# Kernel optimization log

Measured on AMD Instinct MI355X. Metric: run time of the kernel, lower is better.

## Reference

```python
import jax, jax.numpy as jnp
import numpy as np

N_ATOMS, N_EDGES, FEAT, N_RBF, N_CONV = 20000, 320000, 128, 20, 3
CUTOFF = 5.0
ATOM_FEA, H_FEA, N_OUT, VOCAB = 64, 128, 5, 100


def _dense(x, W, b):
    return x @ W + b


def _painn_forward(xyz, embed, W1, b1, W2, b2, Wd, bd, U, V, Ws1, bs1, Ws2, bs2,
                   Wr1, br1, Wr2, br2, Wf1, bf1, Wf2, bf2, Wf3, bf3, z, nbrs):
    act = jax.nn.silu
    i_idx, j_idx = nbrs[:, 0], nbrs[:, 1]          # receiver i, sender j
    r_ij = xyz[j_idx] - xyz[i_idx]                 # [E,3]
    d = jnp.sqrt(jnp.sum(r_ij ** 2, -1) + 1e-12)   # [E]
    unit = r_ij / d[:, None]
    n = jnp.arange(1, N_RBF + 1, dtype=xyz.dtype)
    rbf = jnp.sin(n[None, :] * jnp.pi * d[:, None] / CUTOFF) / d[:, None]   # [E,n_rbf]
    f_cut = 0.5 * (jnp.cos(jnp.pi * d / CUTOFF) + 1.0) * (d < CUTOFF)       # cosine envelope

    s = embed[z]                                   # [N,F]
    v = jnp.zeros((s.shape[0], FEAT, 3), s.dtype)  # [N,F,3]

    for l in range(N_CONV):
        # ---- message block ----
        phi = _dense(act(_dense(s, W1[l], b1[l])), W2[l], b2[l])        # [N,3F]
        w_s = _dense(rbf, Wd[l], bd[l]) * f_cut[:, None]                # [E,3F]
        inv = (phi[j_idx] * w_s).reshape(-1, 3, FEAT)                   # [E,3,F]
        dv_ij = unit[:, None, :] * inv[:, 2, :, None] + inv[:, 0, :, None] * v[j_idx]  # [E,F,3]
        s = s + jax.ops.segment_sum(inv[:, 1, :], i_idx, num_segments=N_ATOMS)
        v = v + jax.ops.segment_sum(dv_ij, i_idx, num_segments=N_ATOMS)
        # ---- update block ----
        u_v = jnp.einsum('nfd,fg->ngd', v, U[l])                        # [N,F,3]
        v_v = jnp.einsum('nfd,fg->ngd', v, V[l])
        v_norm = jnp.sqrt(jnp.sum(v_v ** 2, -1) + 1e-12)                # [N,F]
        split = _dense(act(_dense(jnp.concatenate([s, v_norm], -1), Ws1[l], bs1[l])), Ws2[l], bs2[l])
        a_vv = split[:, :FEAT]
        a_sv = split[:, FEAT:2 * FEAT]
        a_ss = split[:, 2 * FEAT:]
        v = v + u_v * a_vv[:, :, None]
        s = s + jnp.sum(u_v * v_v, -1) * a_sv + a_ss

    # ---- readout (per-atom features) + fully connected head ----
    atom_fea = _dense(act(_dense(s, Wr1, br1)), Wr2, br2)               # [N,atom_fea]
    h = act(_dense(atom_fea, Wf1, bf1))
    h = act(_dense(h, Wf2, bf2))
    return _dense(h, Wf3, bf3)                                          # [N,n_outputs]


def setup_inputs() -> dict:
    key = jax.random.key(0)
    ks = jax.random.split(key, 20)
    sc = 0.08  # ~1/sqrt(feat_dim) to keep activations stable
    def rn(k, shape, s=sc):
        return jax.random.normal(k, shape, dtype=jnp.float32) * s
    return {
        'xyz': jax.random.uniform(ks[0], (N_ATOMS, 3), dtype=jnp.float32) * 4.0,
        'z': jax.random.randint(ks[1], (N_ATOMS,), 0, VOCAB),
        'nbrs': jax.random.randint(ks[2], (N_EDGES, 2), 0, N_ATOMS),
        'embed': rn(ks[3], (VOCAB, FEAT), 1.0),
        'W1': rn(ks[4], (N_CONV, FEAT, FEAT)), 'b1': jnp.zeros((N_CONV, FEAT)),
        'W2': rn(ks[5], (N_CONV, FEAT, 3 * FEAT)), 'b2': jnp.zeros((N_CONV, 3 * FEAT)),
        'Wd': rn(ks[6], (N_CONV, N_RBF, 3 * FEAT)), 'bd': jnp.zeros((N_CONV, 3 * FEAT)),
        'U': rn(ks[7], (N_CONV, FEAT, FEAT)),
        'V': rn(ks[8], (N_CONV, FEAT, FEAT)),
        'Ws1': rn(ks[9], (N_CONV, 2 * FEAT, FEAT)), 'bs1': jnp.zeros((N_CONV, FEAT)),
        'Ws2': rn(ks[10], (N_CONV, FEAT, 3 * FEAT)), 'bs2': jnp.zeros((N_CONV, 3 * FEAT)),
        'Wr1': rn(ks[11], (FEAT, FEAT)), 'br1': jnp.zeros((FEAT,)),
        'Wr2': rn(ks[12], (FEAT, ATOM_FEA)), 'br2': jnp.zeros((ATOM_FEA,)),
        'Wf1': rn(ks[13], (ATOM_FEA, H_FEA)), 'bf1': jnp.zeros((H_FEA,)),
        'Wf2': rn(ks[14], (H_FEA, H_FEA)), 'bf2': jnp.zeros((H_FEA,)),
        'Wf3': rn(ks[15], (H_FEA, N_OUT)), 'bf3': jnp.zeros((N_OUT,)),
    }


def reference(xyz, z, nbrs, embed, W1, b1, W2, b2, Wd, bd, U, V, Ws1, bs1, Ws2, bs2,
              Wr1, br1, Wr2, br2, Wf1, bf1, Wf2, bf2, Wf3, bf3):
    return _painn_forward(xyz, embed, W1, b1, W2, b2, Wd, bd, U, V, Ws1, bs1, Ws2, bs2,
                          Wr1, br1, Wr2, br2, Wf1, bf1, Wf2, bf2, Wf3, bf3, z, nbrs)
```

## Files before the change

kernel.cpp:

```cpp
#include <hip/hip_runtime.h>
#include <hip/hip_bf16.h>
#include <math.h>

#define N_ATOMS 20000
#define N_EDGES 320000
#define FEAT 128
#define N_RBF 20
#define N_CONV 3
#define N_OUT_ 5
#define PI_F 3.14159265358979f
#define M20P 20032
#define M60P 60032

typedef unsigned short ushort;
typedef __bf16 bf16x8 __attribute__((ext_vector_type(8)));
typedef float f32x4 __attribute__((ext_vector_type(4)));

__device__ __forceinline__ float b2f(ushort u){ return __uint_as_float(((unsigned)u) << 16); }
__device__ __forceinline__ ushort f2b(float x){
    unsigned u = __float_as_uint(x);
    return (ushort)((u + 0x7FFFu + ((u >> 16) & 1u)) >> 16);
}
#define MFMA __builtin_amdgcn_mfma_f32_16x16x32_bf16

constexpr size_t rnd64(size_t x){ return (x + 63) & ~size_t(63); }
constexpr size_t F_XYZ  = 64;
constexpr size_t F_EMB  = rnd64(F_XYZ + 60000);
constexpr size_t F_B1   = rnd64(F_EMB + 12800);
constexpr size_t F_B2   = rnd64(F_B1  + 3*128);
constexpr size_t F_WD   = rnd64(F_B2  + 3*384);
constexpr size_t F_BD   = rnd64(F_WD  + 3*20*384);
constexpr size_t F_BS1  = rnd64(F_BD  + 3*384);
constexpr size_t F_BS2  = rnd64(F_BS1 + 3*128);
constexpr size_t F_BR1  = rnd64(F_BS2 + 3*384);
constexpr size_t F_BR2  = rnd64(F_BR1 + 128);
constexpr size_t F_BF1  = rnd64(F_BR2 + 64);
constexpr size_t F_BF2  = rnd64(F_BF1 + 128);
constexpr size_t F_BF3  = rnd64(F_BF2 + 128);
constexpr size_t F_CNT  = rnd64(F_BF3 + 8);
constexpr size_t F_ROW  = rnd64(F_CNT  + N_ATOMS);
constexpr size_t F_CUR  = rnd64(F_ROW  + N_ATOMS + 1);
constexpr size_t F_EID  = rnd64(F_CUR  + N_ATOMS);
constexpr size_t F_EJ   = rnd64(F_EID  + N_EDGES);
constexpr size_t F_EREC = rnd64(F_EJ   + N_EDGES);
constexpr size_t F_S    = rnd64(F_EREC + (size_t)N_EDGES*24);
constexpr size_t F_V    = rnd64(F_S    + (size_t)N_ATOMS*FEAT);
constexpr size_t F_PHI  = rnd64(F_V    + (size_t)60000*FEAT);
constexpr size_t F_VV   = rnd64(F_PHI  + (size_t)N_ATOMS*384);
constexpr size_t F_SPL  = rnd64(F_VV   + (size_t)60000*FEAT);
constexpr size_t F_OUT  = rnd64(F_SPL  + (size_t)N_ATOMS*384);
constexpr size_t H_SHI  = rnd64(F_OUT  + N_ATOMS*N_OUT_);
constexpr size_t H_SLO  = rnd64(H_SHI  + (size_t)M20P*128/2);
constexpr size_t H_VHI  = rnd64(H_SLO  + (size_t)M20P*128/2);
constexpr size_t H_VLO  = rnd64(H_VHI  + (size_t)M60P*128/2);
constexpr size_t H_HAHI = rnd64(H_VLO  + (size_t)M60P*128/2);
constexpr size_t H_HALO = rnd64(H_HAHI + (size_t)M20P*128/2);
constexpr size_t H_HBHI = rnd64(H_HALO + (size_t)M20P*128/2);
constexpr size_t H_HBLO = rnd64(H_HBHI + (size_t)M20P*128/2);
constexpr size_t H_AFHI = rnd64(H_HBLO + (size_t)M20P*128/2);
constexpr size_t H_AFLO = rnd64(H_AFHI + (size_t)M20P*64/2);
constexpr size_t H_WT   = rnd64(H_AFLO + (size_t)M20P*64/2);
constexpr size_t O_W1T=0, O_W2T=49152, O_UT=196608, O_VT=245760, O_WS1T=294912,
                 O_WS2T=393216, O_WR1T=540672, O_WR2T=557056, O_WF1T=565248,
                 O_WF2T=573440, O_WF3T=589824, O_WTOT=598016;

__global__ void k_detect(const unsigned int* __restrict__ bits, int* flag){
    __shared__ int cnt;
    if (threadIdx.x == 0) cnt = 0;
    __syncthreads();
    unsigned int lo = bits[threadIdx.x] & 0xFFFFu;
    if (lo >= 0x3000u && lo <= 0x4100u) atomicAdd(&cnt, 1);
    __syncthreads();
    if (threadIdx.x == 0) *flag = (cnt >= 48) ? 1 : 0;
}

struct P13 { const void* p[13]; };
__global__ void k_cvt_all(P13 sp, float* __restrict__ ws, const int* __restrict__ flag){
    constexpr int   NSEG = 13;
    constexpr int    SZ[NSEG] = {60000,12800,384,1152,23040,1152,384,1152,128,64,128,128,5};
    constexpr size_t DO_[NSEG]= {F_XYZ,F_EMB,F_B1,F_B2,F_WD,F_BD,F_BS1,F_BS2,F_BR1,F_BR2,F_BF1,F_BF2,F_BF3};
    int t = blockIdx.x * blockDim.x + threadIdx.x;
    int bf = *flag;
    #pragma unroll
    for (int s = 0; s < NSEG; s++){
        if (t < SZ[s]){
            float v = bf ? b2f(((const ushort*)sp.p[s])[t]) : ((const float*)sp.p[s])[t];
            ws[DO_[s] + t] = v;
            return;
        }
        t -= SZ[s];
    }
}

struct P11 { const void* p[11]; };
__global__ void k_wt_all(P11 sp, ushort* __restrict__ wb, const int* __restrict__ flag){
    constexpr int NSEG = 23;
    constexpr int SRC[NSEG]  = {0,1,2,3,4,5, 0,1,2,3,4,5, 0,1,2,3,4,5, 6,7,8,9,10};
    constexpr int SOFF[NSEG] = {0,0,0,0,0,0, 16384,49152,16384,16384,32768,49152,
                                32768,98304,32768,32768,65536,98304, 0,0,0,0,0};
    constexpr size_t DOFF[NSEG]={O_W1T,O_W2T,O_UT,O_VT,O_WS1T,O_WS2T,
                                 O_W1T+16384,O_W2T+49152,O_UT+16384,O_VT+16384,O_WS1T+32768,O_WS2T+49152,
                                 O_W1T+32768,O_W2T+98304,O_UT+32768,O_VT+32768,O_WS1T+65536,O_WS2T+98304,
                                 O_WR1T,O_WR2T,O_WF1T,O_WF2T,O_WF3T};
    constexpr int KK[NSEG]   = {128,128,128,128,256,128, 128,128,128,128,256,128,
                                128,128,128,128,256,128, 128,128,64,128,128};
    constexpr int NN[NSEG]   = {128,384,128,128,128,384, 128,384,128,128,128,384,
                                128,384,128,128,128,384, 128,64,128,128,5};
    constexpr int NP[NSEG]   = {128,384,128,128,128,384, 128,384,128,128,128,384,
                                128,384,128,128,128,384, 128,64,128,128,64};
    constexpr int PM[NSEG]   = {0,0,0,0,0,1, 0,0,0,0,0,1, 0,0,0,0,0,1, 0,0,0,0,0};
    int t = blockIdx.x * blockDim.x + threadIdx.x;
    int bf = *flag;
    #pragma unroll
    for (int s = 0; s < NSEG; s++){
        int tot = NP[s] * KK[s];
        if (t < tot){
            int n = t / KK[s], k = t & (KK[s] - 1);
            ushort hi = 0, lo = 0;
            if (n < NN[s]){
                int si = SOFF[s] + k * NN[s] + n;
                float w = bf ? b2f(((const ushort*)sp.p[SRC[s]])[si])
                             : ((const float*)sp.p[SRC[s]])[si];
                hi = f2b(w); lo = f2b(w - b2f(hi));
            }
            int dr = n;
            if (PM[s]) { int g = n & 127, tg = n >> 7; dr = (g >> 6) * 192 + tg * 64 + (g & 63); }
            size_t di = DOFF[s] + (size_t)dr * KK[s] + k;
            wb[di] = hi;
            wb[O_WTOT + di] = lo;
            return;
        }
        t -= tot;
    }
}
constexpr int WT_TOTAL = 598016;

__global__ void k_store_out(const float* __restrict__ src, void* __restrict__ dst, int n,
                            const int* __restrict__ flag){
    int t = blockIdx.x * blockDim.x + threadIdx.x;
    if (t >= n) return;
    float v = src[t];
    if (*flag) ((ushort*)dst)[t] = f2b(v);
    else       ((float*)dst)[t] = v;
}

__global__ void k_zero_f(float* p, int n){
    int t = blockIdx.x * blockDim.x + threadIdx.x;
    if (t < n) p[t] = 0.f;
}
__global__ void k_zero_i(int* p, int n){
    int t = blockIdx.x * blockDim.x + threadIdx.x;
    if (t < n) p[t] = 0;
}
__global__ void k_init_s(const float* __restrict__ embed, const int* __restrict__ z,
                         float* __restrict__ s, ushort* __restrict__ shi,
                         ushort* __restrict__ slo){
    int t = blockIdx.x * blockDim.x + threadIdx.x;
    if (t >= N_ATOMS * FEAT) return;
    int n = t >> 7, f = t & 127;
    float v = embed[z[n] * FEAT + f];
    s[t] = v;
    ushort h = f2b(v); shi[t] = h; slo[t] = f2b(v - b2f(h));
}

__global__ void k_hist(const int* __restrict__ nbrs, int* __restrict__ cnt){
    int e = blockIdx.x * blockDim.x + threadIdx.x;
    if (e < N_EDGES) atomicAdd(&cnt[nbrs[2*e]], 1);
}
__global__ void k_scan(const int* __restrict__ cnt, int* __restrict__ row, int* __restrict__ cur){
    __shared__ int ls[256];
    int t = threadIdx.x, base = t * 80;
    int s = 0;
    for (int k = 0; k < 80; k++){ int i = base + k; if (i < N_ATOMS) s += cnt[i]; }
    ls[t] = s; __syncthreads();
    for (int off = 1; off < 256; off <<= 1){
        int v = (t >= off) ? ls[t - off] : 0;
        __syncthreads();
        ls[t] += v;
        __syncthreads();
    }
    int run = ls[t] - s;
    for (int k = 0; k < 80; k++){
        int i = base + k;
        if (i < N_ATOMS){ row[i] = run; cur[i] = run; run += cnt[i]; }
    }
    if (t == 255) row[N_ATOMS] = ls[255];
}
__global__ void k_fill(const int* __restrict__ nbrs, int* __restrict__ cur, int* __restrict__ eid){
    int e = blockIdx.x * blockDim.x + threadIdx.x;
    if (e >= N_EDGES) return;
    int p = atomicAdd(&cur[nbrs[2*e]], 1);
    eid[p] = e;
}

__global__ void k_geom_csr(const float* __restrict__ xyz, const int* __restrict__ nbrs,
                           const int* __restrict__ eid,
                           int* __restrict__ EJ, float* __restrict__ EREC){
    int idx = blockIdx.x * blockDim.x + threadIdx.x;
    if (idx >= N_EDGES) return;
    int e = eid[idx];
    int i = nbrs[2*e], j = nbrs[2*e+1];
    float rx = xyz[3*j]   - xyz[3*i];
    float ry = xyz[3*j+1] - xyz[3*i+1];
    float rz = xyz[3*j+2] - xyz[3*i+2];
    float d  = sqrtf(rx*rx + ry*ry + rz*rz + 1e-12f);
    float inv = 1.0f / d;
    float b  = PI_F * d * 0.2f;
    float sb = sinf(b), cb = cosf(b);
    float fc = (d < 5.0f) ? 0.5f * (cb + 1.0f) : 0.0f;
    float scale = inv * fc, c2 = 2.0f * cb;
    EJ[idx] = j;
    float* rec = EREC + (size_t)idx * 24;
    rec[0] = fc; rec[1] = rx*inv; rec[2] = ry*inv; rec[3] = rz*inv;
    float sp = 0.f, sc = sb;
    #pragma unroll
    for (int r = 0; r < N_RBF; r++){
        rec[4 + r] = sc * scale;
        float sn = c2 * sc - sp;
        sp = sc; sc = sn;
    }
}

template<int KT>
__global__ __launch_bounds__(256) void k_gemm3t(
    const ushort* __restrict__ Ahi, const ushort* __restrict__ Alo,
    const ushort* __restrict__ Bthi, const ushort* __restrict__ Btlo,
    const float* __restrict__ bias, int M, int N, int act,
    float* __restrict__ Cf, ushort* __restrict__ Chi, ushort* __restrict__ Clo)
{
    int wave = threadIdx.x >> 6, lane = threadIdx.x & 63;
    int l15 = lane & 15, quad = lane >> 4;
    int m0 = blockIdx.y * 128 + wave * 32;
    int n0 = blockIdx.x * 64;
    const ushort* aph = Ahi  + (size_t)(m0 + l15) * KT + quad * 8;
    const ushort* apl = Alo  + (size_t)(m0 + l15) * KT + quad * 8;
    const ushort* bph = Bthi + (size_t)(n0 + l15) * KT + quad * 8;
    const ushort* bpl = Btlo + (size_t)(n0 + l15) * KT + quad * 8;
    f32x4 acc[2][4];
    #pragma unroll
    for (int r = 0; r < 2; r++)
        #pragma unroll
        for (int c = 0; c < 4; c++) acc[r][c] = (f32x4){0.f, 0.f, 0.f, 0.f};
    #pragma unroll
    for (int k0 = 0; k0 < KT; k0 += 32) {
        bf16x8 ah0 = *reinterpret_cast<const bf16x8*>(aph + k0);
        bf16x8 al0 = *reinterpret_cast<const bf16x8*>(apl + k0);
        bf16x8 ah1 = *reinterpret_cast<const bf16x8*>(aph + (size_t)16 * KT + k0);
        bf16x8 al1 = *reinterpret_cast<const bf16x8*>(apl + (size_t)16 * KT + k0);
        #pragma unroll
        for (int c = 0; c < 4; c++) {
            bf16x8 bh = *reinterpret_cast<const bf16x8*>(bph + (size_t)c * 16 * KT + k0);
            bf16x8 bl = *reinterpret_cast<const bf16x8*>(bpl + (size_t)c * 16 * KT + k0);
            acc[0][c] = MFMA(al0, bh, acc[0][c], 0, 0, 0);
            acc[0][c] = MFMA(ah0, bl, acc[0][c], 0, 0, 0);
            acc[0][c] = MFMA(ah0, bh, acc[0][c], 0, 0, 0);
            acc[1][c] = MFMA(al1, bh, acc[1][c], 0, 0, 0);
            acc[1][c] = MFMA(ah1, bl, acc[1][c], 0, 0, 0);
            acc[1][c] = MFMA(ah1, bh, acc[1][c], 0, 0, 0);
        }
    }
    #pragma unroll
    for (int rr = 0; rr < 2; rr++) {
        int row_base = m0 + rr * 16 + quad * 4;
        #pragma unroll
        for (int c = 0; c < 4; c++) {
            int col = n0 + c * 16 + l15;
            #pragma unroll
            for (int r = 0; r < 4; r++) {
                int row = row_base + r;
                if (row < M && col < N) {
                    float v = acc[rr][c][r];
                    if (bias) v += bias[col];
                    if (act)  v = v / (1.f + expf(-v));
                    size_t idx = (size_t)row * N + col;
                    if (Cf)  Cf[idx] = v;
                    if (Chi) { ushort h = f2b(v); Chi[idx] = h; Clo[idx] = f2b(v - b2f(h)); }
                }
            }
        }
    }
}

__global__ __launch_bounds__(256) void k_gemm3_dual(
    const ushort* __restrict__ Ahi, const ushort* __restrict__ Alo,
    const ushort* __restrict__ B1hi, const ushort* __restrict__ B1lo,
    const ushort* __restrict__ B2hi, const ushort* __restrict__ B2lo,
    int M, float* __restrict__ C1, float* __restrict__ C2)
{
    constexpr int KT = 128, N = 128;
    int wave = threadIdx.x >> 6, lane = threadIdx.x & 63;
    int l15 = lane & 15, quad = lane >> 4;
    int m0 = blockIdx.y * 128 + wave * 32;
    int n0 = blockIdx.x * 64;
    const ushort* aph = Ahi  + (size_t)(m0 + l15) * KT + quad * 8;
    const ushort* apl = Alo  + (size_t)(m0 + l15) * KT + quad * 8;
    const ushort* b1h = B1hi + (size_t)(n0 + l15) * KT + quad * 8;
    const ushort* b1l = B1lo + (size_t)(n0 + l15) * KT + quad * 8;
    const ushort* b2h = B2hi + (size_t)(n0 + l15) * KT + quad * 8;
    const ushort* b2l = B2lo + (size_t)(n0 + l15) * KT + quad * 8;
    f32x4 acc1[2][4], acc2[2][4];
    #pragma unroll
    for (int r = 0; r < 2; r++)
        #pragma unroll
        for (int c = 0; c < 4; c++) {
            acc1[r][c] = (f32x4){0.f,0.f,0.f,0.f};
            acc2[r][c] = (f32x4){0.f,0.f,0.f,0.f};
        }
    #pragma unroll
    for (int k0 = 0; k0 < KT; k0 += 32) {
        bf16x8 ah0 = *reinterpret_cast<const bf16x8*>(aph + k0);
        bf16x8 al0 = *reinterpret_cast<const bf16x8*>(apl + k0);
        bf16x8 ah1 = *reinterpret_cast<const bf16x8*>(aph + (size_t)16 * KT + k0);
        bf16x8 al1 = *reinterpret_cast<const bf16x8*>(apl + (size_t)16 * KT + k0);
        #pragma unroll
        for (int c = 0; c < 4; c++) {
            bf16x8 bh = *reinterpret_cast<const bf16x8*>(b1h + (size_t)c * 16 * KT + k0);
            bf16x8 bl = *reinterpret_cast<const bf16x8*>(b1l + (size_t)c * 16 * KT + k0);
            acc1[0][c] = MFMA(al0, bh, acc1[0][c], 0, 0, 0);
            acc1[0][c] = MFMA(ah0, bl, acc1[0][c], 0, 0, 0);
            acc1[0][c] = MFMA(ah0, bh, acc1[0][c], 0, 0, 0);
            acc1[1][c] = MFMA(al1, bh, acc1[1][c], 0, 0, 0);
            acc1[1][c] = MFMA(ah1, bl, acc1[1][c], 0, 0, 0);
            acc1[1][c] = MFMA(ah1, bh, acc1[1][c], 0, 0, 0);
        }
        #pragma unroll
        for (int c = 0; c < 4; c++) {
            bf16x8 bh = *reinterpret_cast<const bf16x8*>(b2h + (size_t)c * 16 * KT + k0);
            bf16x8 bl = *reinterpret_cast<const bf16x8*>(b2l + (size_t)c * 16 * KT + k0);
            acc2[0][c] = MFMA(al0, bh, acc2[0][c], 0, 0, 0);
            acc2[0][c] = MFMA(ah0, bl, acc2[0][c], 0, 0, 0);
            acc2[0][c] = MFMA(ah0, bh, acc2[0][c], 0, 0, 0);
            acc2[1][c] = MFMA(al1, bh, acc2[1][c], 0, 0, 0);
            acc2[1][c] = MFMA(ah1, bl, acc2[1][c], 0, 0, 0);
            acc2[1][c] = MFMA(ah1, bh, acc2[1][c], 0, 0, 0);
        }
    }
    #pragma unroll
    for (int rr = 0; rr < 2; rr++) {
        int row_base = m0 + rr * 16 + quad * 4;
        #pragma unroll
        for (int c = 0; c < 4; c++) {
            int col = n0 + c * 16 + l15;
            #pragma unroll
            for (int r = 0; r < 4; r++) {
                int row = row_base + r;
                if (row < M) {
                    size_t idx = (size_t)row * N + col;
                    C1[idx] = acc1[rr][c][r];
                    C2[idx] = acc2[rr][c][r];
                }
            }
        }
    }
}

__global__ __launch_bounds__(384) void k_ws2up(
    const ushort* __restrict__ Ahi, const ushort* __restrict__ Alo,
    const ushort* __restrict__ Bphi, const ushort* __restrict__ Bplo,
    const float* __restrict__ bs2,
    const float* __restrict__ uv, const float* __restrict__ vvf,
    const ushort* __restrict__ vhi, const ushort* __restrict__ vlo,
    float* __restrict__ s, float* __restrict__ v,
    ushort* __restrict__ shi, ushort* __restrict__ slo, int M)
{
    constexpr int KT = 128, LDG = 200;
    __shared__ float gl[64 * LDG];
    int wave = threadIdx.x >> 6, lane = threadIdx.x & 63;
    int l15 = lane & 15, quad = lane >> 4;
    int tg = wave >> 1, rh = wave & 1;
    int m0 = blockIdx.y * 64 + rh * 32;
    int X  = blockIdx.x;
    const ushort* aph = Ahi  + (size_t)(m0 + l15) * KT + quad * 8;
    const ushort* apl = Alo  + (size_t)(m0 + l15) * KT + quad * 8;
    const ushort* bph = Bphi + (size_t)(X * 192 + tg * 64 + l15) * KT + quad * 8;
    const ushort* bpl = Bplo + (size_t)(X * 192 + tg * 64 + l15) * KT + quad * 8;
    f32x4 acc[2][4];
    #pragma unroll
    for (int r = 0; r < 2; r++)
        #pragma unroll
        for (int c = 0; c < 4; c++) acc[r][c] = (f32x4){0.f, 0.f, 0.f, 0.f};
    #pragma unroll
    for (int k0 = 0; k0 < KT; k0 += 32) {
        bf16x8 ah0 = *reinterpret_cast<const bf16x8*>(aph + k0);
        bf16x8 al0 = *reinterpret_cast<const bf16x8*>(apl + k0);
        bf16x8 ah1 = *reinterpret_cast<const bf16x8*>(aph + (size_t)16 * KT + k0);
        bf16x8 al1 = *reinterpret_cast<const bf16x8*>(apl + (size_t)16 * KT + k0);
        #pragma unroll
        for (int c = 0; c < 4; c++) {
            bf16x8 bh = *reinterpret_cast<const bf16x8*>(bph + (size_t)c * 16 * KT + k0);
            bf16x8 bl = *reinterpret_cast<const bf16x8*>(bpl + (size_t)c * 16 * KT + k0);
            acc[0][c] = MFMA(al0, bh, acc[0][c], 0, 0, 0);
            acc[0][c] = MFMA(ah0, bl, acc[0][c], 0, 0, 0);
            acc[0][c] = MFMA(ah0, bh, acc[0][c], 0, 0, 0);
            acc[1][c] = MFMA(al1, bh, acc[1][c], 0, 0, 0);
            acc[1][c] = MFMA(ah1, bl, acc[1][c], 0, 0, 0);
            acc[1][c] = MFMA(ah1, bh, acc[1][c], 0, 0, 0);
        }
    }
    #pragma unroll
    for (int rr = 0; rr < 2; rr++) {
        #pragma unroll
        for (int c = 0; c < 4; c++) {
            #pragma unroll
            for (int r = 0; r < 4; r++) {
                int lrow = rh * 32 + rr * 16 + quad * 4 + r;
                int gc   = c * 16 + l15;
                gl[lrow * LDG + tg * 64 + gc] = acc[rr][c][r] + bs2[tg * 128 + X * 64 + gc];
            }
        }
    }
    __syncthreads();
    int a0 = blockIdx.y * 64;
    for (int t = threadIdx.x; t < 64 * 64; t += 384) {
        int al = t >> 6, gc = t & 63;
        int a = a0 + al;
        if (a >= M) continue;
        int g = X * 64 + gc;
        float avv = gl[al * LDG + gc];
        float asv = gl[al * LDG + 64 + gc];
        float ass = gl[al * LDG + 128 + gc];
        size_t b = (size_t)a * 384 + g;
        float dot = 0.f;
        #pragma unroll
        for (int d = 0; d < 3; d++) {
            size_t idx = b + (size_t)d * 128;
            float u  = uv[idx];
            float w  = vvf[idx];
            float vb = b2f(vhi[idx]) + b2f(vlo[idx]);
            dot = fmaf(u, w, dot);
            v[idx] = vb + u * avv;
        }
        size_t st = (size_t)a * FEAT + g;
        float ns = s[st] + dot * asv + ass;
        s[st] = ns;
        ushort h = f2b(ns); shi[st] = h; slo[st] = f2b(ns - b2f(h));
    }
}

__global__ __launch_bounds__(128) void k_edge4(
    const float* __restrict__ phi, const float* __restrict__ vin,
    const int* __restrict__ EJ, const float* __restrict__ EREC,
    const int* __restrict__ row,
    const float* __restrict__ Wd, const float* __restrict__ bd,
    float* __restrict__ s, ushort* __restrict__ vhi, ushort* __restrict__ vlo)
{
    int i = blockIdx.x, f = threadIdx.x;
    float wdr[3 * N_RBF];
    #pragma unroll
    for (int r = 0; r < N_RBF; r++) {
        wdr[r]           = Wd[r*384 + f];
        wdr[N_RBF + r]   = Wd[r*384 + 128 + f];
        wdr[2*N_RBF + r] = Wd[r*384 + 256 + f];
    }
    float bd0 = bd[f], bd1 = bd[128 + f], bd2 = bd[256 + f];
    float sacc = 0.f, va0 = 0.f, va1 = 0.f, va2 = 0.f;
    int beg = row[i], end = row[i + 1];

    auto body = [&](int idx){
        int j = EJ[idx];
        const float4* rq = reinterpret_cast<const float4*>(EREC + (size_t)idx * 24);
        float4 q0 = rq[0], q1 = rq[1], q2 = rq[2], q3 = rq[3], q4 = rq[4], q5 = rq[5];
        float g[20] = {q1.x,q1.y,q1.z,q1.w, q2.x,q2.y,q2.z,q2.w,
                       q3.x,q3.y,q3.z,q3.w, q4.x,q4.y,q4.z,q4.w,
                       q5.x,q5.y,q5.z,q5.w};
        float w0 = bd0 * q0.x, w1 = bd1 * q0.x, w2 = bd2 * q0.x;
        #pragma unroll
        for (int r = 0; r < N_RBF; r++) {
            w0 = fmaf(g[r], wdr[r],           w0);
            w1 = fmaf(g[r], wdr[N_RBF + r],   w1);
            w2 = fmaf(g[r], wdr[2*N_RBF + r], w2);
        }
        size_t pj = (size_t)j * 384;
        float inv0 = phi[pj + f]       * w0;
        float inv1 = phi[pj + 128 + f] * w1;
        float inv2 = phi[pj + 256 + f] * w2;
        size_t vj = (size_t)j * 384 + f;
        sacc += inv1;
        va0 = fmaf(inv0, vin[vj],       fmaf(q0.y, inv2, va0));
        va1 = fmaf(inv0, vin[vj + 128], fmaf(q0.z, inv2, va1));
        va2 = fmaf(inv0, vin[vj + 256], fmaf(q0.w, inv2, va2));
    };

    int idx = beg;
    for (; idx + 1 < end; idx += 2) { body(idx); body(idx + 1); }
    if (idx < end) body(idx);

    s[(size_t)i * FEAT + f] += sacc;
    size_t vi = (size_t)i * 384 + f;
    float n0 = vin[vi] + va0, n1 = vin[vi + 128] + va1, n2 = vin[vi + 256] + va2;
    ushort h;
    h = f2b(n0); vhi[vi]       = h; vlo[vi]       = f2b(n0 - b2f(h));
    h = f2b(n1); vhi[vi + 128] = h; vlo[vi + 128] = f2b(n1 - b2f(h));
    h = f2b(n2); vhi[vi + 256] = h; vlo[vi + 256] = f2b(n2 - b2f(h));
}

__global__ void k_vnorm_cat(const float* __restrict__ s, const float* __restrict__ vv,
                            ushort* __restrict__ chi, ushort* __restrict__ clo){
    int t = blockIdx.x * blockDim.x + threadIdx.x;
    if (t >= N_ATOMS * FEAT) return;
    int n = t >> 7, g = t & 127;
    size_t b = (size_t)n * 384 + g;
    float a0 = vv[b], a1 = vv[b + 128], a2 = vv[b + 256];
    float nr = sqrtf(a0*a0 + a1*a1 + a2*a2 + 1e-12f);
    float sv = s[t];
    size_t c0 = (size_t)n * 256 + g;
    ushort h;
    h = f2b(sv); chi[c0]       = h; clo[c0]       = f2b(sv - b2f(h));
    h = f2b(nr); chi[c0 + 128] = h; clo[c0 + 128] = f2b(nr - b2f(h));
}

struct Pair { ushort* hi; ushort* lo; };

static inline void gemm3(Pair A, Pair B, const float* bias,
                         int M, int K, int N, int Npad, int act,
                         float* Cf, Pair C, hipStream_t s){
    dim3 g(Npad / 64, (M + 127) / 128), b(256);
    switch (K) {
    case 64:  k_gemm3t<64> <<<g, b, 0, s>>>(A.hi, A.lo, B.hi, B.lo, bias, M, N, act, Cf, C.hi, C.lo); break;
    case 128: k_gemm3t<128><<<g, b, 0, s>>>(A.hi, A.lo, B.hi, B.lo, bias, M, N, act, Cf, C.hi, C.lo); break;
    case 256: k_gemm3t<256><<<g, b, 0, s>>>(A.hi, A.lo, B.hi, B.lo, bias, M, N, act, Cf, C.hi, C.lo); break;
    }
}

extern "C" void kernel_launch(void* const* d_in, const int* in_sizes, int n_in,
                              void* d_out, int out_size, void* d_ws, size_t ws_size,
                              hipStream_t stream) {
    float* ws = (float*)d_ws;
    int* flag = (int*)d_ws;
    const int* z    = (const int*)d_in[1];
    const int* nbrs = (const int*)d_in[2];

    k_detect<<<1, 64, 0, stream>>>((const unsigned int*)d_in[0], flag);

    P13 cp; {
        const int cidx[13] = {0,3,5,7,8,9,13,15,17,19,21,23,25};
        for (int i = 0; i < 13; i++) cp.p[i] = d_in[cidx[i]];
    }
    k_cvt_all<<<(100517 + 255)/256, 256, 0, stream>>>(cp, ws, flag);

    ushort* wb = (ushort*)(ws + H_WT);
    P11 wp; {
        const int widx[11] = {4,6,10,11,12,14,16,18,20,22,24};
        for (int i = 0; i < 11; i++) wp.p[i] = d_in[widx[i]];
    }
    k_wt_all<<<(WT_TOTAL + 255)/256, 256, 0, stream>>>(wp, wb, flag);

    int* cnt = (int*)(ws + F_CNT); int* row = (int*)(ws + F_ROW);
    int* cur = (int*)(ws + F_CUR); int* eid = (int*)(ws + F_EID);
    int* EJ  = (int*)(ws + F_EJ);  float* EREC = ws + F_EREC;
    k_zero_i<<<(N_ATOMS+255)/256, 256, 0, stream>>>(cnt, N_ATOMS);
    k_hist<<<(N_EDGES+255)/256, 256, 0, stream>>>(nbrs, cnt);
    k_scan<<<1, 256, 0, stream>>>(cnt, row, cur);
    k_fill<<<(N_EDGES+255)/256, 256, 0, stream>>>(nbrs, cur, eid);
    k_geom_csr<<<(N_EDGES+255)/256, 256, 0, stream>>>(ws + F_XYZ, nbrs, eid, EJ, EREC);

    float* S   = ws + F_S;
    float* V   = ws + F_V;
    float* PHI = ws + F_PHI;
    float* VV  = ws + F_VV;
    Pair SHL { (ushort*)(ws + H_SHI),  (ushort*)(ws + H_SLO)  };
    Pair VHL { (ushort*)(ws + H_VHI),  (ushort*)(ws + H_VLO)  };
    Pair HA  { (ushort*)(ws + H_HAHI), (ushort*)(ws + H_HALO) };
    Pair HB  { (ushort*)(ws + H_HBHI), (ushort*)(ws + H_HBLO) };
    Pair AF  { (ushort*)(ws + H_AFHI), (ushort*)(ws + H_AFLO) };
    Pair CAT { (ushort*)(ws + F_SPL),  (ushort*)(ws + F_SPL) + (size_t)M20P*256 };
    Pair NOP { nullptr, nullptr };

    k_init_s<<<(N_ATOMS*FEAT+255)/256, 256, 0, stream>>>(ws + F_EMB, z, S, SHL.hi, SHL.lo);
    k_zero_f<<<(60000*FEAT+255)/256, 256, 0, stream>>>(V, 60000*FEAT);

    for (int l = 0; l < N_CONV; l++) {
        gemm3(SHL, Pair{wb + O_W1T + l*16384, wb + O_WTOT + O_W1T + l*16384},
              ws + F_B1 + l*128, N_ATOMS, 128, 128, 128, 1, nullptr, HA, stream);
        gemm3(HA, Pair{wb + O_W2T + l*49152, wb + O_WTOT + O_W2T + l*49152},
              ws + F_B2 + l*384, N_ATOMS, 128, 384, 384, 0, PHI, NOP, stream);
        k_edge4<<<N_ATOMS, 128, 0, stream>>>(PHI, V, EJ, EREC, row,
                                             ws + F_WD + (size_t)l*20*384, ws + F_BD + l*384,
                                             S, VHL.hi, VHL.lo);
        {
            dim3 g(2, (60000 + 127) / 128), b(256);
            k_gemm3_dual<<<g, b, 0, stream>>>(VHL.hi, VHL.lo,
                                              wb + O_UT + l*16384, wb + O_WTOT + O_UT + l*16384,
                                              wb + O_VT + l*16384, wb + O_WTOT + O_VT + l*16384,
                                              60000, PHI, VV);
        }
        k_vnorm_cat<<<(N_ATOMS*FEAT+255)/256, 256, 0, stream>>>(S, VV, CAT.hi, CAT.lo);
        gemm3(CAT, Pair{wb + O_WS1T + l*32768, wb + O_WTOT + O_WS1T + l*32768},
              ws + F_BS1 + l*128, N_ATOMS, 256, 128, 128, 1, nullptr, HB, stream);
        {
            dim3 g(2, (N_ATOMS + 63) / 64), b(384);
            k_ws2up<<<g, b, 0, stream>>>(HB.hi, HB.lo,
                                         wb + O_WS2T + l*49152, wb + O_WTOT + O_WS2T + l*49152,
                                         ws + F_BS2 + l*384,
                                         PHI, VV, VHL.hi, VHL.lo,
                                         S, V, SHL.hi, SHL.lo, N_ATOMS);
        }
    }

    gemm3(SHL, Pair{wb + O_WR1T, wb + O_WTOT + O_WR1T}, ws + F_BR1,
          N_ATOMS, 128, 128, 128, 1, nullptr, HA, stream);
    gemm3(HA,  Pair{wb + O_WR2T, wb + O_WTOT + O_WR2T}, ws + F_BR2,
          N_ATOMS, 128,  64,  64, 0, nullptr, AF, stream);
    gemm3(AF,  Pair{wb + O_WF1T, wb + O_WTOT + O_WF1T}, ws + F_BF1,
          N_ATOMS,  64, 128, 128, 1, nullptr, HB, stream);
    gemm3(HB,  Pair{wb + O_WF2T, wb + O_WTOT + O_WF2T}, ws + F_BF2,
          N_ATOMS, 128, 128, 128, 1, nullptr, HA, stream);
    gemm3(HA,  Pair{wb + O_WF3T, wb + O_WTOT + O_WF3T}, ws + F_BF3,
          N_ATOMS, 128, N_OUT_, 64, 0, ws + F_OUT, NOP, stream);

    k_store_out<<<(N_ATOMS*N_OUT_+255)/256, 256, 0, stream>>>(ws + F_OUT, d_out, N_ATOMS*N_OUT_, flag);
}
```

Baseline: 1.343 ms.

## Fuse vector-norm/concat into dual U/V GEMM and skip zero-v reads on first layer

The dual U/V GEMM now tiles rows in steps of 126, so each block holds whole atoms (42 atoms of 3 rows). It stages the V-projection tile in shared memory and computes the per-atom vector norm plus the split bf16 concat with s inline, which removes the separate k_vnorm_cat pass and its reread of VV. The edge kernel is templated so the first layer skips reading the all-zero v, which also removes the zeroing kernel. The cost is overlapping tiles (128 rows computed per 126 used), some wasted MFMA work, a larger padded V buffer, and 35KB of shared memory per block.

```diff
diff --git a/kernel.cpp b/kernel.cpp
--- a/kernel.cpp
+++ b/kernel.cpp
@@ -10,7 +10,7 @@
 #define N_OUT_ 5
 #define PI_F 3.14159265358979f
 #define M20P 20032
-#define M60P 60032
+#define M60PAD 60160
 
 typedef unsigned short ushort;
 typedef __bf16 bf16x8 __attribute__((ext_vector_type(8)));
@@ -52,8 +52,8 @@
 constexpr size_t H_SHI  = rnd64(F_OUT  + N_ATOMS*N_OUT_);
 constexpr size_t H_SLO  = rnd64(H_SHI  + (size_t)M20P*128/2);
 constexpr size_t H_VHI  = rnd64(H_SLO  + (size_t)M20P*128/2);
-constexpr size_t H_VLO  = rnd64(H_VHI  + (size_t)M60P*128/2);
-constexpr size_t H_HAHI = rnd64(H_VLO  + (size_t)M60P*128/2);
+constexpr size_t H_VLO  = rnd64(H_VHI  + (size_t)M60PAD*128/2);
+constexpr size_t H_HAHI = rnd64(H_VLO  + (size_t)M60PAD*128/2);
 constexpr size_t H_HALO = rnd64(H_HAHI + (size_t)M20P*128/2);
 constexpr size_t H_HBHI = rnd64(H_HALO + (size_t)M20P*128/2);
 constexpr size_t H_HBLO = rnd64(H_HBHI + (size_t)M20P*128/2);
@@ -144,10 +144,6 @@
     else       ((float*)dst)[t] = v;
 }
 
-__global__ void k_zero_f(float* p, int n){
-    int t = blockIdx.x * blockDim.x + threadIdx.x;
-    if (t < n) p[t] = 0.f;
-}
 __global__ void k_zero_i(int* p, int n){
     int t = blockIdx.x * blockDim.x + threadIdx.x;
     if (t < n) p[t] = 0;
@@ -281,16 +277,19 @@
     }
 }
 
-__global__ __launch_bounds__(256) void k_gemm3_dual(
+__global__ __launch_bounds__(256) void k_dual_vn(
     const ushort* __restrict__ Ahi, const ushort* __restrict__ Alo,
     const ushort* __restrict__ B1hi, const ushort* __restrict__ B1lo,
     const ushort* __restrict__ B2hi, const ushort* __restrict__ B2lo,
-    int M, float* __restrict__ C1, float* __restrict__ C2)
+    const float* __restrict__ s,
+    float* __restrict__ C1, float* __restrict__ C2,
+    ushort* __restrict__ chi, ushort* __restrict__ clo)
 {
-    constexpr int KT = 128, N = 128;
+    constexpr int KT = 128, N = 128, MROWS = 60000, LDV = 68;
+    __shared__ float vvs[128 * LDV];
     int wave = threadIdx.x >> 6, lane = threadIdx.x & 63;
     int l15 = lane & 15, quad = lane >> 4;
-    int m0 = blockIdx.y * 128 + wave * 32;
+    int m0 = blockIdx.y * 126 + wave * 32;
     int n0 = blockIdx.x * 64;
     const ushort* aph = Ahi  + (size_t)(m0 + l15) * KT + quad * 8;
     const ushort* apl = Alo  + (size_t)(m0 + l15) * KT + quad * 8;
@@ -337,20 +336,39 @@
     }
     #pragma unroll
     for (int rr = 0; rr < 2; rr++) {
-        int row_base = m0 + rr * 16 + quad * 4;
         #pragma unroll
         for (int c = 0; c < 4; c++) {
             int col = n0 + c * 16 + l15;
             #pragma unroll
             for (int r = 0; r < 4; r++) {
-                int row = row_base + r;
-                if (row < M) {
+                int lrow = wave * 32 + rr * 16 + quad * 4 + r;
+                int row  = m0 + rr * 16 + quad * 4 + r;
+                float vv = acc2[rr][c][r];
+                vvs[lrow * LDV + c * 16 + l15] = vv;
+                if (row < MROWS) {
                     size_t idx = (size_t)row * N + col;
                     C1[idx] = acc1[rr][c][r];
-                    C2[idx] = acc2[rr][c][r];
+                    C2[idx] = vv;
                 }
             }
         }
+    }
+    __syncthreads();
+    int a0 = blockIdx.y * 42;
+    for (int t = threadIdx.x; t < 42 * 64; t += 256) {
+        int a_loc = t >> 6, c = t & 63;
+        int a = a0 + a_loc;
+        if (a >= N_ATOMS) continue;
+        float v0 = vvs[(a_loc * 3 + 0) * LDV + c];
+        float v1 = vvs[(a_loc * 3 + 1) * LDV + c];
+        float v2 = vvs[(a_loc * 3 + 2) * LDV + c];
+        float nr = sqrtf(v0 * v0 + v1 * v1 + v2 * v2 + 1e-12f);
+        int g = n0 + c;
+        float sv = s[(size_t)a * FEAT + g];
+        size_t c0 = (size_t)a * 256 + g;
+        ushort h;
+        h = f2b(sv); chi[c0]       = h; clo[c0]       = f2b(sv - b2f(h));
+        h = f2b(nr); chi[c0 + 128] = h; clo[c0 + 128] = f2b(nr - b2f(h));
     }
 }
 
@@ -437,7 +455,8 @@
     }
 }
 
-__global__ __launch_bounds__(128) void k_edge4(
+template<int FIRST>
+__global__ __launch_bounds__(128) void k_edge4t(
     const float* __restrict__ phi, const float* __restrict__ vin,
     const int* __restrict__ EJ, const float* __restrict__ EREC,
     const int* __restrict__ row,
@@ -474,11 +493,17 @@
         float inv0 = phi[pj + f]       * w0;
         float inv1 = phi[pj + 128 + f] * w1;
         float inv2 = phi[pj + 256 + f] * w2;
-        size_t vj = (size_t)j * 384 + f;
         sacc += inv1;
-        va0 = fmaf(inv0, vin[vj],       fmaf(q0.y, inv2, va0));
-        va1 = fmaf(inv0, vin[vj + 128], fmaf(q0.z, inv2, va1));
-        va2 = fmaf(inv0, vin[vj + 256], fmaf(q0.w, inv2, va2));
+        if (FIRST) {
+            va0 = fmaf(q0.y, inv2, va0);
+            va1 = fmaf(q0.z, inv2, va1);
+            va2 = fmaf(q0.w, inv2, va2);
+        } else {
+            size_t vj = (size_t)j * 384 + f;
+            va0 = fmaf(inv0, vin[vj],       fmaf(q0.y, inv2, va0));
+            va1 = fmaf(inv0, vin[vj + 128], fmaf(q0.z, inv2, va1));
+            va2 = fmaf(inv0, vin[vj + 256], fmaf(q0.w, inv2, va2));
+        }
     };
 
     int idx = beg;
@@ -487,26 +512,13 @@
 
     s[(size_t)i * FEAT + f] += sacc;
     size_t vi = (size_t)i * 384 + f;
-    float n0 = vin[vi] + va0, n1 = vin[vi + 128] + va1, n2 = vin[vi + 256] + va2;
+    float n0, n1, n2;
+    if (FIRST) { n0 = va0; n1 = va1; n2 = va2; }
+    else { n0 = vin[vi] + va0; n1 = vin[vi + 128] + va1; n2 = vin[vi + 256] + va2; }
     ushort h;
     h = f2b(n0); vhi[vi]       = h; vlo[vi]       = f2b(n0 - b2f(h));
     h = f2b(n1); vhi[vi + 128] = h; vlo[vi + 128] = f2b(n1 - b2f(h));
     h = f2b(n2); vhi[vi + 256] = h; vlo[vi + 256] = f2b(n2 - b2f(h));
-}
-
-__global__ void k_vnorm_cat(const float* __restrict__ s, const float* __restrict__ vv,
-                            ushort* __restrict__ chi, ushort* __restrict__ clo){
-    int t = blockIdx.x * blockDim.x + threadIdx.x;
-    if (t >= N_ATOMS * FEAT) return;
-    int n = t >> 7, g = t & 127;
-    size_t b = (size_t)n * 384 + g;
-    float a0 = vv[b], a1 = vv[b + 128], a2 = vv[b + 256];
-    float nr = sqrtf(a0*a0 + a1*a1 + a2*a2 + 1e-12f);
-    float sv = s[t];
-    size_t c0 = (size_t)n * 256 + g;
-    ushort h;
-    h = f2b(sv); chi[c0]       = h; clo[c0]       = f2b(sv - b2f(h));
-    h = f2b(nr); chi[c0 + 128] = h; clo[c0 + 128] = f2b(nr - b2f(h));
 }
 
 struct Pair { ushort* hi; ushort* lo; };
@@ -567,24 +579,25 @@
     Pair NOP { nullptr, nullptr };
 
     k_init_s<<<(N_ATOMS*FEAT+255)/256, 256, 0, stream>>>(ws + F_EMB, z, S, SHL.hi, SHL.lo);
-    k_zero_f<<<(60000*FEAT+255)/256, 256, 0, stream>>>(V, 60000*FEAT);
 
     for (int l = 0; l < N_CONV; l++) {
         gemm3(SHL, Pair{wb + O_W1T + l*16384, wb + O_WTOT + O_W1T + l*16384},
               ws + F_B1 + l*128, N_ATOMS, 128, 128, 128, 1, nullptr, HA, stream);
         gemm3(HA, Pair{wb + O_W2T + l*49152, wb + O_WTOT + O_W2T + l*49152},
               ws + F_B2 + l*384, N_ATOMS, 128, 384, 384, 0, PHI, NOP, stream);
-        k_edge4<<<N_ATOMS, 128, 0, stream>>>(PHI, V, EJ, EREC, row,
-                                             ws + F_WD + (size_t)l*20*384, ws + F_BD + l*384,
-                                             S, VHL.hi, VHL.lo);
+        if (l == 0)
+            k_edge4t<1><<<N_ATOMS, 128, 0, stream>>>(PHI, V, EJ, EREC, row,
+                ws + F_WD + (size_t)l*20*384, ws + F_BD + l*384, S, VHL.hi, VHL.lo);
+        else
+            k_edge4t<0><<<N_ATOMS, 128, 0, stream>>>(PHI, V, EJ, EREC, row,
+                ws + F_WD + (size_t)l*20*384, ws + F_BD + l*384, S, VHL.hi, VHL.lo);
         {
-            dim3 g(2, (60000 + 127) / 128), b(256);
-            k_gemm3_dual<<<g, b, 0, stream>>>(VHL.hi, VHL.lo,
-                                              wb + O_UT + l*16384, wb + O_WTOT + O_UT + l*16384,
-                                              wb + O_VT + l*16384, wb + O_WTOT + O_VT + l*16384,
-                                              60000, PHI, VV);
-        }
-        k_vnorm_cat<<<(N_ATOMS*FEAT+255)/256, 256, 0, stream>>>(S, VV, CAT.hi, CAT.lo);
+            dim3 g(2, 477), b(256);
+            k_dual_vn<<<g, b, 0, stream>>>(VHL.hi, VHL.lo,
+                                           wb + O_UT + l*16384, wb + O_WTOT + O_UT + l*16384,
+                                           wb + O_VT + l*16384, wb + O_WTOT + O_VT + l*16384,
+                                           S, PHI, VV, CAT.hi, CAT.lo);
+        }
         gemm3(CAT, Pair{wb + O_WS1T + l*32768, wb + O_WTOT + O_WS1T + l*32768},
               ws + F_BS1 + l*128, N_ATOMS, 256, 128, 128, 1, nullptr, HB, stream);
         {
```

Measured after the change: 1.263 ms, median of 2. -5.9%, faster.
